# Optimization experiments

Hardware: AMD Instinct MI355X
Metric: run time of the kernel (lower is better)

The kernel has to match this reference:

```python
import jax, jax.numpy as jnp
import numpy as np

N_QUBITS = 4 + 4  # 8
N_LAYERS = 4
DIM = 2 ** N_QUBITS


def _apply_1q(state, U, wire):
    # state: (B, 2,...,2) complex; U: (2,2) complex; contract qubit `wire`
    s = jnp.moveaxis(state, wire + 1, -1)
    s = s @ U.T  # out[..., i] = sum_j U[i, j] * s[..., j]
    return jnp.moveaxis(s, -1, wire + 1)


def _apply_cnot(state, c, t):
    s = jnp.moveaxis(state, (c + 1, t + 1), (-2, -1))  # (..., 2c, 2t)
    s = jnp.concatenate([s[..., 0:1, :], s[..., 1:2, ::-1]], axis=-2)
    return jnp.moveaxis(s, (-2, -1), (c + 1, t + 1))


def _quantum_layer(q_in, qw):
    """Batched statevector sim: RY(pi*x) encoding + StronglyEntanglingLayers + <Z_i>."""
    B = q_in.shape[0]
    # RY(a)|0> = cos(a/2)|0> + sin(a/2)|1>, a = pi * x  -> product state
    half = q_in * (jnp.pi / 2)
    qvecs = jnp.stack([jnp.cos(half), jnp.sin(half)], axis=-1).astype(jnp.complex64)  # (B, n, 2)
    state = qvecs[:, 0]
    for i in range(1, N_QUBITS):
        state = (state[:, :, None] * qvecs[:, i][:, None, :]).reshape(B, -1)
    state = state.reshape((B,) + (2,) * N_QUBITS)
    # Rot(phi, theta, omega) = RZ(omega) RY(theta) RZ(phi)
    phi, theta, omega = qw[..., 0], qw[..., 1], qw[..., 2]
    c, s = jnp.cos(theta / 2), jnp.sin(theta / 2)
    m00 = jnp.exp(-0.5j * (phi + omega)) * c
    m01 = -jnp.exp(0.5j * (phi - omega)) * s
    m10 = jnp.exp(-0.5j * (phi - omega)) * s
    m11 = jnp.exp(0.5j * (phi + omega)) * c
    rot = jnp.stack([jnp.stack([m00, m01], -1), jnp.stack([m10, m11], -1)], -2)  # (L, n, 2, 2)
    rot = rot.astype(jnp.complex64)
    for l in range(N_LAYERS):
        for w in range(N_QUBITS):
            state = _apply_1q(state, rot[l, w], w)
        r = (l % (N_QUBITS - 1)) + 1  # PennyLane default ranges
        for w in range(N_QUBITS):
            state = _apply_cnot(state, w, (w + r) % N_QUBITS)
    amps = state.reshape(B, DIM)
    probs = jnp.real(amps * jnp.conj(amps))  # (B, 2^n) float32
    # <Z_i> = sum_b probs_b * (+1 if bit_i(b)==0 else -1); wire 0 = most significant axis
    idx = np.arange(DIM)
    bits = (idx[None, :] >> (N_QUBITS - 1 - np.arange(N_QUBITS))[:, None]) & 1  # (n, 2^n)
    zvals = jnp.asarray(1.0 - 2.0 * bits, dtype=jnp.float32)
    return probs @ zvals.T  # (B, n)


def _forward(x, w_pre1, b_pre1, w_pre2, b_pre2, w_pre3, b_pre3, qw,
             w_post1, b_post1, w_post2, b_post2, w_post3, b_post3):
    # eval mode: dropout is identity
    h = jax.nn.relu(x @ w_pre1 + b_pre1)
    h = jax.nn.relu(h @ w_pre2 + b_pre2)
    q_in = jnp.tanh(h @ w_pre3 + b_pre3)          # (B, n_qubits)
    z = _quantum_layer(q_in, qw)                   # (B, n_qubits)
    h = jax.nn.relu(z @ w_post1 + b_post1)
    h = jax.nn.relu(h @ w_post2 + b_post2)
    return h @ w_post3 + b_post3                   # (B, num_classes)


def setup_inputs() -> dict:
    key = jax.random.key(0)
    ks = jax.random.split(key, 16)
    B, D_IN, C = 16384, 41, 5
    def lin(k, fan_in, fan_out):
        lim = 1.0 / np.sqrt(fan_in)
        k1, k2 = jax.random.split(k)
        return (jax.random.uniform(k1, (fan_in, fan_out), jnp.float32, -lim, lim),
                jax.random.uniform(k2, (fan_out,), jnp.float32, -lim, lim))
    x = jax.random.normal(ks[0], (B, D_IN), jnp.float32)
    w_pre1, b_pre1 = lin(ks[1], D_IN, 64)
    w_pre2, b_pre2 = lin(ks[2], 64, 32)
    w_pre3, b_pre3 = lin(ks[3], 32, N_QUBITS)
    qw = jax.random.normal(ks[4], (N_LAYERS, N_QUBITS, 3), jnp.float32) * 0.1
    w_post1, b_post1 = lin(ks[5], N_QUBITS, 32)
    w_post2, b_post2 = lin(ks[6], 32, 16)
    w_post3, b_post3 = lin(ks[7], 16, C)
    return dict(x=x, w_pre1=w_pre1, b_pre1=b_pre1, w_pre2=w_pre2, b_pre2=b_pre2,
                w_pre3=w_pre3, b_pre3=b_pre3, qw=qw,
                w_post1=w_post1, b_post1=b_post1, w_post2=w_post2, b_post2=b_post2,
                w_post3=w_post3, b_post3=b_post3)


def reference(x, w_pre1, b_pre1, w_pre2, b_pre2, w_pre3, b_pre3, qw,
              w_post1, b_post1, w_post2, b_post2, w_post3, b_post3):
    return _forward(x, w_pre1, b_pre1, w_pre2, b_pre2, w_pre3, b_pre3, qw,
                    w_post1, b_post1, w_post2, b_post2, w_post3, b_post3)
```

## Files before the change

### kernel.cpp

```cpp
#include <hip/hip_runtime.h>
#include <math.h>

#define PI_HALF 1.57079632679489662f

typedef float v2f __attribute__((ext_vector_type(2)));
typedef unsigned uv2 __attribute__((ext_vector_type(2)));


__device__ __forceinline__ v2f sp(float x) { v2f r; r.x = x; r.y = x; return r; }
__device__ __forceinline__ v2f pkfma(v2f a, v2f b, v2f c) {
  return __builtin_elementwise_fma(a, b, c);
}

template <int CTRL>
__device__ __forceinline__ float dpp_mov(float v) {
  int r = __builtin_amdgcn_update_dpp(0, __float_as_int(v), CTRL, 0xf, 0xf, true);
  return __int_as_float(r);
}

template <int MASK>
__device__ __forceinline__ float lane_xor(float v, bool odd) {
  if constexpr (MASK == 1) return dpp_mov<0xB1>(v);
  else if constexpr (MASK == 2) return dpp_mov<0x4E>(v);
  else if constexpr (MASK == 4) return dpp_mov<0x1B>(dpp_mov<0x141>(v));
  else if constexpr (MASK == 8) return dpp_mov<0x128>(v);
  else {
#if __has_builtin(__builtin_amdgcn_permlane16_swap)
    uv2 r = __builtin_amdgcn_permlane16_swap(__float_as_uint(v),
                                             __float_as_uint(v), false, false);
    return __uint_as_float(odd ? r.x : r.y);
#else
    return __int_as_float(__builtin_amdgcn_ds_swizzle(__float_as_int(v), 0x401F));
#endif
  }
}
template <int MASK>
__device__ __forceinline__ v2f dpp2(v2f v, bool odd) {
  v2f r; r.x = lane_xor<MASK>(v.x, odd); r.y = lane_xor<MASK>(v.y, odd);
  return r;
}

template <int W>
__device__ __forceinline__ void rot_lane(v2f (&RE)[4], v2f (&IM)[4],
                                         const float4 mA, int g) {
  constexpr int LM = 1 << (4 - W);
  const bool odd = (g >> 4) & 1;
  const unsigned bit = (g >> (4 - W)) & 1u;
  const int sgn = (int)(bit << 31);
  v2f Av = sp(mA.x);
  v2f Bv = sp(__int_as_float(__float_as_int(mA.y) ^ sgn));
  v2f Cv = sp(__int_as_float(__float_as_int(mA.z) ^ sgn));
  v2f Dv = sp(mA.w);
#pragma unroll
  for (int j = 0; j < 4; ++j) {
    v2f pr = dpp2<LM>(RE[j], odd);
    v2f pi = dpp2<LM>(IM[j], odd);
    v2f nr = pkfma(-Dv, pi, pkfma(Cv, pr, pkfma(-Bv, IM[j], Av * RE[j])));
    v2f ni = pkfma( Dv, pr, pkfma(Cv, pi, pkfma( Bv, RE[j], Av * IM[j])));
    RE[j] = nr; IM[j] = ni;
  }
}

template <int JM>
__device__ __forceinline__ void rot_regj(v2f (&RE)[4], v2f (&IM)[4],
                                         const float4 mA) {
  v2f M0r = sp(mA.x), M0i = sp(mA.y), M1r = sp(mA.z), M1i = sp(mA.w);
#pragma unroll
  for (int j = 0; j < 4; ++j) {
    if (!(j & JM)) {
      const int j1 = j | JM;
      v2f r0 = RE[j], i0 = IM[j], r1 = RE[j1], i1 = IM[j1];
      RE[j]  = pkfma(-M1i, i1, pkfma(M1r, r1, pkfma(-M0i, i0, M0r * r0)));
      IM[j]  = pkfma( M1i, r1, pkfma(M1r, i1, pkfma( M0i, r0, M0r * i0)));
      RE[j1] = pkfma( M0i, i1, pkfma(M0r, r1, pkfma(-M1i, i0, (-M1r) * r0)));
      IM[j1] = pkfma(-M0i, r1, pkfma(M0r, i1, pkfma( M1i, r0, (-M1r) * i0)));
    }
  }
}

__device__ __forceinline__ void rot_regh(v2f (&RE)[4], v2f (&IM)[4],
                                         const float4 mA) {
#pragma unroll
  for (int j = 0; j < 4; ++j) {
    float r0 = RE[j].x, i0 = IM[j].x, r1 = RE[j].y, i1 = IM[j].y;
    RE[j].x = fmaf(-mA.w, i1, fmaf(mA.z, r1, fmaf(-mA.y, i0, mA.x * r0)));
    IM[j].x = fmaf( mA.w, r1, fmaf(mA.z, i1, fmaf( mA.y, r0, mA.x * i0)));
    RE[j].y = fmaf( mA.y, i1, fmaf(mA.x, r1, fmaf(-mA.w, i0, -mA.z * r0)));
    IM[j].y = fmaf(-mA.y, r1, fmaf(mA.x, i1, fmaf( mA.w, r0, -mA.z * i0)));
  }
}

template <int GPOS, int LM>
__device__ __forceinline__ void cnot_LL(v2f (&RE)[4], v2f (&IM)[4], int g) {
  const bool cb = (g >> GPOS) & 1;
  const bool odd = (g >> 4) & 1;
#pragma unroll
  for (int j = 0; j < 4; ++j) {
    v2f pr = dpp2<LM>(RE[j], odd);
    v2f pi = dpp2<LM>(IM[j], odd);
    RE[j] = cb ? pr : RE[j];
    IM[j] = cb ? pi : IM[j];
  }
}
template <int GPOS, int JM>
__device__ __forceinline__ void cnot_LR(v2f (&RE)[4], v2f (&IM)[4], int g) {
  const bool cb = (g >> GPOS) & 1;
#pragma unroll
  for (int j = 0; j < 4; ++j) {
    if (!(j & JM)) {
      const int j1 = j | JM;
      v2f r0 = RE[j], r1 = RE[j1];
      RE[j] = cb ? r1 : r0;  RE[j1] = cb ? r0 : r1;
      v2f i0 = IM[j], i1 = IM[j1];
      IM[j] = cb ? i1 : i0;  IM[j1] = cb ? i0 : i1;
    }
  }
}
template <int GPOS>
__device__ __forceinline__ void cnot_LH(v2f (&RE)[4], v2f (&IM)[4], int g) {
  const bool cb = (g >> GPOS) & 1;
#pragma unroll
  for (int j = 0; j < 4; ++j) {
    v2f r = RE[j]; v2f rs; rs.x = r.y; rs.y = r.x;
    RE[j] = cb ? rs : r;
    v2f i = IM[j]; v2f is2; is2.x = i.y; is2.y = i.x;
    IM[j] = cb ? is2 : i;
  }
}
template <int JC, int LM>
__device__ __forceinline__ void cnot_RL(v2f (&RE)[4], v2f (&IM)[4], int g) {
  const bool odd = (g >> 4) & 1;
#pragma unroll
  for (int j = 0; j < 4; ++j) {
    if (j & JC) {
      RE[j] = dpp2<LM>(RE[j], odd);
      IM[j] = dpp2<LM>(IM[j], odd);
    }
  }
}
template <int JC>
__device__ __forceinline__ void cnot_RH(v2f (&RE)[4], v2f (&IM)[4]) {
#pragma unroll
  for (int j = 0; j < 4; ++j) {
    if (j & JC) {
      v2f r = RE[j]; RE[j].x = r.y; RE[j].y = r.x;
      v2f i = IM[j]; IM[j].x = i.y; IM[j].y = i.x;
    }
  }
}
template <int LM>
__device__ __forceinline__ void cnot_HL(v2f (&RE)[4], v2f (&IM)[4], int g) {
  const bool odd = (g >> 4) & 1;
#pragma unroll
  for (int j = 0; j < 4; ++j) {
    RE[j].y = lane_xor<LM>(RE[j].y, odd);
    IM[j].y = lane_xor<LM>(IM[j].y, odd);
  }
}
template <int JC, int JT>
__device__ __forceinline__ void cnot_RR(v2f (&RE)[4], v2f (&IM)[4]) {
#pragma unroll
  for (int j = 0; j < 4; ++j) {
    if ((j & JC) && !(j & JT)) {
      const int j1 = j | JT;
      v2f t = RE[j]; RE[j] = RE[j1]; RE[j1] = t;
      t = IM[j]; IM[j] = IM[j1]; IM[j1] = t;
    }
  }
}

__device__ __forceinline__ void stage_fence() { __threadfence_block(); }

__global__ __launch_bounds__(256) void hqc_kernel(
    const float* __restrict__ x,
    const float* __restrict__ w1, const float* __restrict__ b1,
    const float* __restrict__ w2, const float* __restrict__ b2,
    const float* __restrict__ w3, const float* __restrict__ b3,
    const float* __restrict__ qw,
    const float* __restrict__ wp1, const float* __restrict__ bp1,
    const float* __restrict__ wp2, const float* __restrict__ bp2,
    const float* __restrict__ wp3, const float* __restrict__ bp3,
    float* __restrict__ out, int B) {
  __shared__ __align__(16) float rotm[32][4];
  __shared__ float xbuf[8][44];
  __shared__ __align__(16) float hbuf[8][68];
  __shared__ float h2buf[8][34];
  __shared__ float qbuf[8][20];
  __shared__ float p1buf[8][34];
  __shared__ float p2buf[8][20];

  const int tid = threadIdx.x;
  const int g = tid & 31;
  const int ls = tid >> 5;
  const int s = blockIdx.x * 8 + ls;
  const bool valid = (s < B);

  if (tid < 32) {
    float phi = qw[tid * 3 + 0];
    float th  = qw[tid * 3 + 1];
    float om  = qw[tid * 3 + 2];
    float st_, ct; sincosf(0.5f * th, &st_, &ct);
    float sa, ca;  sincosf(0.5f * (phi + om), &sa, &ca);
    float sb, cb;  sincosf(0.5f * (phi - om), &sb, &cb);
    rotm[tid][0] =  ca * ct;
    rotm[tid][1] = -sa * ct;
    rotm[tid][2] = -cb * st_;
    rotm[tid][3] = -sb * st_;
  }

  if (valid) {
    xbuf[ls][g] = x[s * 41 + g];
    if (g < 9) xbuf[ls][g + 32] = x[s * 41 + g + 32];
  }
  __syncthreads();

  const v2f* w1v = (const v2f*)w1;
  v2f a1 = ((const v2f*)b1)[g];
#pragma unroll 8
  for (int k = 0; k < 41; ++k)
    a1 = pkfma(sp(xbuf[ls][k]), w1v[k * 32 + g], a1);
  v2f st2; st2.x = fmaxf(a1.x, 0.f); st2.y = fmaxf(a1.y, 0.f);
  *(v2f*)(&hbuf[ls][2 * g]) = st2;
  stage_fence();

  float a2 = b2[g];
#pragma unroll 8
  for (int k = 0; k < 64; ++k) a2 = fmaf(hbuf[ls][k], w2[k * 32 + g], a2);
  h2buf[ls][g] = fmaxf(a2, 0.f);
  stage_fence();

  if (g < 8) {
    float acc = b3[g];
#pragma unroll
    for (int k = 0; k < 32; ++k) acc = fmaf(h2buf[ls][k], w3[k * 8 + g], acc);
    float q = tanhf(acc);
    float sh, ch; sincosf(q * PI_HALF, &sh, &ch);
    qbuf[ls][g]     = ch;
    qbuf[ls][8 + g] = sh;
  }
  stage_fence();

  float cwv[8], swv[8];
#pragma unroll
  for (int w = 0; w < 8; ++w) { cwv[w] = qbuf[ls][w]; swv[w] = qbuf[ls][8 + w]; }
  float lp = 1.0f;
#pragma unroll
  for (int w = 0; w < 5; ++w) lp *= ((g >> (4 - w)) & 1) ? swv[w] : cwv[w];
  float f56[4];
#pragma unroll
  for (int a = 0; a < 4; ++a)
    f56[a] = ((a & 2) ? swv[5] : cwv[5]) * ((a & 1) ? swv[6] : cwv[6]);
  v2f F7; F7.x = cwv[7]; F7.y = swv[7];
  v2f RE[4], IM[4];
#pragma unroll
  for (int j = 0; j < 4; ++j) {
    RE[j] = sp(lp * f56[j]) * F7;
    IM[j] = sp(0.0f);
  }

#define RM(L, W) (*(const float4*)(&rotm[(L) * 8 + (W)][0]))
#define ROTS(L)                          \
  rot_lane<0>(RE, IM, RM(L, 0), g);      \
  rot_lane<1>(RE, IM, RM(L, 1), g);      \
  rot_lane<2>(RE, IM, RM(L, 2), g);      \
  rot_lane<3>(RE, IM, RM(L, 3), g);      \
  rot_lane<4>(RE, IM, RM(L, 4), g);      \
  rot_regj<2>(RE, IM, RM(L, 5));         \
  rot_regj<1>(RE, IM, RM(L, 6));         \
  rot_regh(RE, IM, RM(L, 7));

  ROTS(0)
  cnot_LL<4, 8>(RE, IM, g);  cnot_LL<3, 4>(RE, IM, g);
  cnot_LL<2, 2>(RE, IM, g);  cnot_LL<1, 1>(RE, IM, g);
  cnot_LR<0, 2>(RE, IM, g);  cnot_RR<2, 1>(RE, IM);
  cnot_RH<1>(RE, IM);        cnot_HL<16>(RE, IM, g);
  ROTS(1)
  cnot_LL<4, 4>(RE, IM, g);  cnot_LL<3, 2>(RE, IM, g);
  cnot_LL<2, 1>(RE, IM, g);  cnot_LR<1, 2>(RE, IM, g);
  cnot_LR<0, 1>(RE, IM, g);  cnot_RH<2>(RE, IM);
  cnot_RL<1, 16>(RE, IM, g); cnot_HL<8>(RE, IM, g);
  ROTS(2)
  cnot_LL<4, 2>(RE, IM, g);  cnot_LL<3, 1>(RE, IM, g);
  cnot_LR<2, 2>(RE, IM, g);  cnot_LR<1, 1>(RE, IM, g);
  cnot_LH<0>(RE, IM, g);     cnot_RL<2, 16>(RE, IM, g);
  cnot_RL<1, 8>(RE, IM, g);  cnot_HL<4>(RE, IM, g);
  ROTS(3)
  cnot_LL<4, 1>(RE, IM, g);  cnot_LR<3, 2>(RE, IM, g);
  cnot_LR<2, 1>(RE, IM, g);  cnot_LH<1>(RE, IM, g);
  cnot_LL<0, 16>(RE, IM, g); cnot_RL<2, 8>(RE, IM, g);
  cnot_RL<1, 4>(RE, IM, g);  cnot_HL<2>(RE, IM, g);

  v2f pv[4];
#pragma unroll
  for (int j = 0; j < 4; ++j) pv[j] = pkfma(RE[j], RE[j], IM[j] * IM[j]);
  v2f tv = (pv[0] + pv[1]) + (pv[2] + pv[3]);
  float tot = tv.x + tv.y;
  v2f v5 = pv[2] + pv[3]; float s5 = v5.x + v5.y;
  v2f v6 = pv[1] + pv[3]; float s6 = v6.x + v6.y;
  float s7 = tv.y;
  float zp[8];
  zp[0] = ((g >> 4) & 1) ? -tot : tot;
  zp[1] = ((g >> 3) & 1) ? -tot : tot;
  zp[2] = ((g >> 2) & 1) ? -tot : tot;
  zp[3] = ((g >> 1) & 1) ? -tot : tot;
  zp[4] = (g & 1) ? -tot : tot;
  zp[5] = fmaf(-2.f, s5, tot);
  zp[6] = fmaf(-2.f, s6, tot);
  zp[7] = fmaf(-2.f, s7, tot);
  {
    const bool odd = (g >> 4) & 1;
#pragma unroll
    for (int w = 0; w < 8; ++w) zp[w] += lane_xor<1>(zp[w], odd);
#pragma unroll
    for (int w = 0; w < 8; ++w) zp[w] += lane_xor<2>(zp[w], odd);
#pragma unroll
    for (int w = 0; w < 8; ++w) zp[w] += lane_xor<4>(zp[w], odd);
#pragma unroll
    for (int w = 0; w < 8; ++w) zp[w] += lane_xor<8>(zp[w], odd);
#pragma unroll
    for (int w = 0; w < 8; ++w) zp[w] += lane_xor<16>(zp[w], odd);
  }

  float q1 = bp1[g];
#pragma unroll
  for (int k = 0; k < 8; ++k) q1 = fmaf(zp[k], wp1[k * 32 + g], q1);
  p1buf[ls][g] = fmaxf(q1, 0.f);
  stage_fence();

  if (g < 16) {
    float q2 = bp2[g];
#pragma unroll
    for (int k = 0; k < 32; ++k) q2 = fmaf(p1buf[ls][k], wp2[k * 16 + g], q2);
    p2buf[ls][g] = fmaxf(q2, 0.f);
  }
  stage_fence();

  if (g < 5 && valid) {
    float o = bp3[g];
#pragma unroll
    for (int k = 0; k < 16; ++k) o = fmaf(p2buf[ls][k], wp3[k * 5 + g], o);
    out[s * 5 + g] = o;
  }
}

extern "C" void kernel_launch(void* const* d_in, const int* in_sizes, int n_in,
                              void* d_out, int out_size, void* d_ws,
                              size_t ws_size, hipStream_t stream) {
  const float* x   = (const float*)d_in[0];
  const float* w1  = (const float*)d_in[1];
  const float* b1  = (const float*)d_in[2];
  const float* w2  = (const float*)d_in[3];
  const float* b2  = (const float*)d_in[4];
  const float* w3  = (const float*)d_in[5];
  const float* b3  = (const float*)d_in[6];
  const float* qw  = (const float*)d_in[7];
  const float* wp1 = (const float*)d_in[8];
  const float* bp1 = (const float*)d_in[9];
  const float* wp2 = (const float*)d_in[10];
  const float* bp2 = (const float*)d_in[11];
  const float* wp3 = (const float*)d_in[12];
  const float* bp3 = (const float*)d_in[13];
  float* out = (float*)d_out;
  const int B = in_sizes[0] / 41;
  const int blocks = (B + 7) / 8;
  hipLaunchKernelGGL(hqc_kernel, dim3(blocks), dim3(256), 0, stream,
                     x, w1, b1, w2, b2, w3, b3, qw,
                     wp1, bp1, wp2, bp2, wp3, bp3, out, B);
}
```

Baseline: 51.72 us.

## Interleave sample pairs in LDS for packed MLP and use masked DPP CNOTs

Shared buffers now interleave the two samples held by each wavefront, so the pre-MLP layers run packed FMAs across two samples, each lane taking one output column (64 wide in layer 1). Controlled-NOTs whose control and target both sit in lane bits now use DPP row/bank write masks, or a single quad permute, in place of a permute followed by a select. Rotation coefficients are loaded before the rotation sequence begins. This is meant to cut VALU select instructions and scalar FMAs, in exchange for more involved DPP mask encodings that must match the qubit mapping exactly.

New measurement: 49.69 us. -3.9%, faster.

```diff
diff --git a/kernel.cpp b/kernel.cpp
--- a/kernel.cpp
+++ b/kernel.cpp
@@ -16,6 +16,22 @@
 __device__ __forceinline__ float dpp_mov(float v) {
   int r = __builtin_amdgcn_update_dpp(0, __float_as_int(v), CTRL, 0xf, 0xf, true);
   return __int_as_float(r);
+}
+template <int CTRL, int ROW, int BANK>
+__device__ __forceinline__ float mdpp(float old_, float src) {
+  int r = __builtin_amdgcn_update_dpp(__float_as_int(old_), __float_as_int(src),
+                                      CTRL, ROW, BANK, false);
+  return __int_as_float(r);
+}
+
+__device__ __forceinline__ float xor16f(float v, bool odd) {
+#if __has_builtin(__builtin_amdgcn_permlane16_swap)
+  uv2 r = __builtin_amdgcn_permlane16_swap(__float_as_uint(v),
+                                           __float_as_uint(v), false, false);
+  return __uint_as_float(odd ? r.x : r.y);
+#else
+  return __int_as_float(__builtin_amdgcn_ds_swizzle(__float_as_int(v), 0x401F));
+#endif
 }
 
 template <int MASK>
@@ -24,15 +40,7 @@
   else if constexpr (MASK == 2) return dpp_mov<0x4E>(v);
   else if constexpr (MASK == 4) return dpp_mov<0x1B>(dpp_mov<0x141>(v));
   else if constexpr (MASK == 8) return dpp_mov<0x128>(v);
-  else {
-#if __has_builtin(__builtin_amdgcn_permlane16_swap)
-    uv2 r = __builtin_amdgcn_permlane16_swap(__float_as_uint(v),
-                                             __float_as_uint(v), false, false);
-    return __uint_as_float(odd ? r.x : r.y);
-#else
-    return __int_as_float(__builtin_amdgcn_ds_swizzle(__float_as_int(v), 0x401F));
-#endif
-  }
+  else return xor16f(v, odd);
 }
 template <int MASK>
 __device__ __forceinline__ v2f dpp2(v2f v, bool odd) {
@@ -90,16 +98,49 @@
   }
 }
 
-template <int GPOS, int LM>
-__device__ __forceinline__ void cnot_LL(v2f (&RE)[4], v2f (&IM)[4], int g) {
+template <int CTRL, int ROW, int BANK>
+__device__ __forceinline__ void cnot_mask(v2f (&RE)[4], v2f (&IM)[4]) {
+#pragma unroll
+  for (int j = 0; j < 4; ++j) {
+    RE[j].x = mdpp<CTRL, ROW, BANK>(RE[j].x, RE[j].x);
+    RE[j].y = mdpp<CTRL, ROW, BANK>(RE[j].y, RE[j].y);
+    IM[j].x = mdpp<CTRL, ROW, BANK>(IM[j].x, IM[j].x);
+    IM[j].y = mdpp<CTRL, ROW, BANK>(IM[j].y, IM[j].y);
+  }
+}
+template <int ROW, int BANK>
+__device__ __forceinline__ void cnot_mask4(v2f (&RE)[4], v2f (&IM)[4]) {
+#pragma unroll
+  for (int j = 0; j < 4; ++j) {
+    float t0 = dpp_mov<0x141>(RE[j].x);
+    float t1 = dpp_mov<0x141>(RE[j].y);
+    float t2 = dpp_mov<0x141>(IM[j].x);
+    float t3 = dpp_mov<0x141>(IM[j].y);
+    RE[j].x = mdpp<0x1B, ROW, BANK>(RE[j].x, t0);
+    RE[j].y = mdpp<0x1B, ROW, BANK>(RE[j].y, t1);
+    IM[j].x = mdpp<0x1B, ROW, BANK>(IM[j].x, t2);
+    IM[j].y = mdpp<0x1B, ROW, BANK>(IM[j].y, t3);
+  }
+}
+__device__ __forceinline__ void cnot_quadB4(v2f (&RE)[4], v2f (&IM)[4]) {
+#pragma unroll
+  for (int j = 0; j < 4; ++j) {
+    RE[j].x = dpp_mov<0xB4>(RE[j].x);
+    RE[j].y = dpp_mov<0xB4>(RE[j].y);
+    IM[j].x = dpp_mov<0xB4>(IM[j].x);
+    IM[j].y = dpp_mov<0xB4>(IM[j].y);
+  }
+}
+template <int GPOS>
+__device__ __forceinline__ void cnot_LL16(v2f (&RE)[4], v2f (&IM)[4], int g) {
   const bool cb = (g >> GPOS) & 1;
   const bool odd = (g >> 4) & 1;
 #pragma unroll
   for (int j = 0; j < 4; ++j) {
-    v2f pr = dpp2<LM>(RE[j], odd);
-    v2f pi = dpp2<LM>(IM[j], odd);
-    RE[j] = cb ? pr : RE[j];
-    IM[j] = cb ? pi : IM[j];
+    float a = xor16f(RE[j].x, odd), b = xor16f(RE[j].y, odd);
+    float c = xor16f(IM[j].x, odd), d = xor16f(IM[j].y, odd);
+    RE[j].x = cb ? a : RE[j].x;  RE[j].y = cb ? b : RE[j].y;
+    IM[j].x = cb ? c : IM[j].x;  IM[j].y = cb ? d : IM[j].y;
   }
 }
 template <int GPOS, int JM>
@@ -121,30 +162,40 @@
   const bool cb = (g >> GPOS) & 1;
 #pragma unroll
   for (int j = 0; j < 4; ++j) {
-    v2f r = RE[j]; v2f rs; rs.x = r.y; rs.y = r.x;
-    RE[j] = cb ? rs : r;
-    v2f i = IM[j]; v2f is2; is2.x = i.y; is2.y = i.x;
-    IM[j] = cb ? is2 : i;
-  }
-}
-template <int JC, int LM>
+    float rx = RE[j].x, ix = IM[j].x;
+    RE[j].x = cb ? RE[j].y : rx;  RE[j].y = cb ? rx : RE[j].y;
+    IM[j].x = cb ? IM[j].y : ix;  IM[j].y = cb ? ix : IM[j].y;
+  }
+}
+template <int JSEL, int LM>
 __device__ __forceinline__ void cnot_RL(v2f (&RE)[4], v2f (&IM)[4], int g) {
   const bool odd = (g >> 4) & 1;
 #pragma unroll
   for (int j = 0; j < 4; ++j) {
-    if (j & JC) {
+    if (j & JSEL) {
       RE[j] = dpp2<LM>(RE[j], odd);
       IM[j] = dpp2<LM>(IM[j], odd);
     }
   }
 }
-template <int JC>
+template <int JSEL>
+__device__ __forceinline__ void cnot_RL16(v2f (&RE)[4], v2f (&IM)[4], int g) {
+  const bool odd = (g >> 4) & 1;
+#pragma unroll
+  for (int j = 0; j < 4; ++j) {
+    if (j & JSEL) {
+      RE[j].x = xor16f(RE[j].x, odd);  RE[j].y = xor16f(RE[j].y, odd);
+      IM[j].x = xor16f(IM[j].x, odd);  IM[j].y = xor16f(IM[j].y, odd);
+    }
+  }
+}
+template <int JSEL>
 __device__ __forceinline__ void cnot_RH(v2f (&RE)[4], v2f (&IM)[4]) {
 #pragma unroll
   for (int j = 0; j < 4; ++j) {
-    if (j & JC) {
-      v2f r = RE[j]; RE[j].x = r.y; RE[j].y = r.x;
-      v2f i = IM[j]; IM[j].x = i.y; IM[j].y = i.x;
+    if (j & JSEL) {
+      float t = RE[j].x; RE[j].x = RE[j].y; RE[j].y = t;
+      t = IM[j].x; IM[j].x = IM[j].y; IM[j].y = t;
     }
   }
 }
@@ -155,6 +206,14 @@
   for (int j = 0; j < 4; ++j) {
     RE[j].y = lane_xor<LM>(RE[j].y, odd);
     IM[j].y = lane_xor<LM>(IM[j].y, odd);
+  }
+}
+__device__ __forceinline__ void cnot_HL16(v2f (&RE)[4], v2f (&IM)[4], int g) {
+  const bool odd = (g >> 4) & 1;
+#pragma unroll
+  for (int j = 0; j < 4; ++j) {
+    RE[j].y = xor16f(RE[j].y, odd);
+    IM[j].y = xor16f(IM[j].y, odd);
   }
 }
 template <int JC, int JT>
@@ -182,17 +241,19 @@
     const float* __restrict__ wp3, const float* __restrict__ bp3,
     float* __restrict__ out, int B) {
   __shared__ __align__(16) float rotm[32][4];
-  __shared__ float xbuf[8][44];
-  __shared__ __align__(16) float hbuf[8][68];
-  __shared__ float h2buf[8][34];
-  __shared__ float qbuf[8][20];
-  __shared__ float p1buf[8][34];
-  __shared__ float p2buf[8][20];
+  __shared__ __align__(8) float xp[4][41][2];
+  __shared__ __align__(8) float hp[4][64][2];
+  __shared__ __align__(8) float h2p[4][32][2];
+  __shared__ __align__(8) float qb[4][16][2];
+  __shared__ __align__(8) float p1p[4][32][2];
+  __shared__ __align__(8) float p2p[4][16][2];
 
   const int tid = threadIdx.x;
+  const int lane = tid & 63;
+  const int wv = tid >> 6;
+  const int half = (tid >> 5) & 1;
   const int g = tid & 31;
-  const int ls = tid >> 5;
-  const int s = blockIdx.x * 8 + ls;
+  const int s = blockIdx.x * 8 + (tid >> 5);
   const bool valid = (s < B);
 
   if (tid < 32) {
@@ -209,40 +270,54 @@
   }
 
   if (valid) {
-    xbuf[ls][g] = x[s * 41 + g];
-    if (g < 9) xbuf[ls][g + 32] = x[s * 41 + g + 32];
+    xp[wv][g][half] = x[s * 41 + g];
+    if (g < 9) xp[wv][g + 32][half] = x[s * 41 + 32 + g];
   }
   __syncthreads();
 
-  const v2f* w1v = (const v2f*)w1;
-  v2f a1 = ((const v2f*)b1)[g];
+  {
+    const int col = lane;
+    v2f acc = sp(b1[col]);
 #pragma unroll 8
-  for (int k = 0; k < 41; ++k)
-    a1 = pkfma(sp(xbuf[ls][k]), w1v[k * 32 + g], a1);
-  v2f st2; st2.x = fmaxf(a1.x, 0.f); st2.y = fmaxf(a1.y, 0.f);
-  *(v2f*)(&hbuf[ls][2 * g]) = st2;
+    for (int k = 0; k < 41; ++k) {
+      v2f xk = *(const v2f*)&xp[wv][k][0];
+      acc = pkfma(xk, sp(w1[k * 64 + col]), acc);
+    }
+    acc.x = fmaxf(acc.x, 0.f); acc.y = fmaxf(acc.y, 0.f);
+    *(v2f*)&hp[wv][col][0] = acc;
+  }
   stage_fence();
 
-  float a2 = b2[g];
+  {
+    v2f acc = sp(b2[g]);
 #pragma unroll 8
-  for (int k = 0; k < 64; ++k) a2 = fmaf(hbuf[ls][k], w2[k * 32 + g], a2);
-  h2buf[ls][g] = fmaxf(a2, 0.f);
+    for (int k = 0; k < 64; ++k) {
+      v2f hk = *(const v2f*)&hp[wv][k][0];
+      acc = pkfma(hk, sp(w2[k * 32 + g]), acc);
+    }
+    acc.x = fmaxf(acc.x, 0.f); acc.y = fmaxf(acc.y, 0.f);
+    if (half == 0) *(v2f*)&h2p[wv][g][0] = acc;
+  }
   stage_fence();
 
   if (g < 8) {
     float acc = b3[g];
 #pragma unroll
-    for (int k = 0; k < 32; ++k) acc = fmaf(h2buf[ls][k], w3[k * 8 + g], acc);
+    for (int k = 0; k < 32; ++k)
+      acc = fmaf(h2p[wv][k][half], w3[k * 8 + g], acc);
     float q = tanhf(acc);
     float sh, ch; sincosf(q * PI_HALF, &sh, &ch);
-    qbuf[ls][g]     = ch;
-    qbuf[ls][8 + g] = sh;
+    qb[wv][g][half]     = ch;
+    qb[wv][8 + g][half] = sh;
   }
   stage_fence();
 
   float cwv[8], swv[8];
 #pragma unroll
-  for (int w = 0; w < 8; ++w) { cwv[w] = qbuf[ls][w]; swv[w] = qbuf[ls][8 + w]; }
+  for (int w = 0; w < 8; ++w) {
+    cwv[w] = qb[wv][w][half];
+    swv[w] = qb[wv][8 + w][half];
+  }
   float lp = 1.0f;
 #pragma unroll
   for (int w = 0; w < 5; ++w) lp *= ((g >> (4 - w)) & 1) ? swv[w] : cwv[w];
@@ -259,36 +334,56 @@
   }
 
 #define RM(L, W) (*(const float4*)(&rotm[(L) * 8 + (W)][0]))
-#define ROTS(L)                          \
-  rot_lane<0>(RE, IM, RM(L, 0), g);      \
-  rot_lane<1>(RE, IM, RM(L, 1), g);      \
-  rot_lane<2>(RE, IM, RM(L, 2), g);      \
-  rot_lane<3>(RE, IM, RM(L, 3), g);      \
-  rot_lane<4>(RE, IM, RM(L, 4), g);      \
-  rot_regj<2>(RE, IM, RM(L, 5));         \
-  rot_regj<1>(RE, IM, RM(L, 6));         \
-  rot_regh(RE, IM, RM(L, 7));
+#define ROTS(L)                                                          \
+  {                                                                      \
+    float4 c0 = RM(L, 0), c1 = RM(L, 1), c2 = RM(L, 2), c3 = RM(L, 3),   \
+           c4 = RM(L, 4), c5 = RM(L, 5), c6 = RM(L, 6), c7 = RM(L, 7);   \
+    rot_lane<0>(RE, IM, c0, g);                                          \
+    rot_lane<1>(RE, IM, c1, g);                                          \
+    rot_lane<2>(RE, IM, c2, g);                                          \
+    rot_lane<3>(RE, IM, c3, g);                                          \
+    rot_lane<4>(RE, IM, c4, g);                                          \
+    rot_regj<2>(RE, IM, c5);                                             \
+    rot_regj<1>(RE, IM, c6);                                             \
+    rot_regh(RE, IM, c7);                                                \
+  }
 
   ROTS(0)
-  cnot_LL<4, 8>(RE, IM, g);  cnot_LL<3, 4>(RE, IM, g);
-  cnot_LL<2, 2>(RE, IM, g);  cnot_LL<1, 1>(RE, IM, g);
-  cnot_LR<0, 2>(RE, IM, g);  cnot_RR<2, 1>(RE, IM);
-  cnot_RH<1>(RE, IM);        cnot_HL<16>(RE, IM, g);
+  cnot_mask<0x128, 0xA, 0xF>(RE, IM);
+  cnot_mask4<0xF, 0xC>(RE, IM);
+  cnot_mask<0x4E, 0xF, 0xA>(RE, IM);
+  cnot_quadB4(RE, IM);
+  cnot_LR<0, 2>(RE, IM, g);
+  cnot_RR<2, 1>(RE, IM);
+  cnot_RH<1>(RE, IM);
+  cnot_HL16(RE, IM, g);
   ROTS(1)
-  cnot_LL<4, 4>(RE, IM, g);  cnot_LL<3, 2>(RE, IM, g);
-  cnot_LL<2, 1>(RE, IM, g);  cnot_LR<1, 2>(RE, IM, g);
-  cnot_LR<0, 1>(RE, IM, g);  cnot_RH<2>(RE, IM);
-  cnot_RL<1, 16>(RE, IM, g); cnot_HL<8>(RE, IM, g);
+  cnot_mask4<0xA, 0xF>(RE, IM);
+  cnot_mask<0x4E, 0xF, 0xC>(RE, IM);
+  cnot_mask<0xB1, 0xF, 0xA>(RE, IM);
+  cnot_LR<1, 2>(RE, IM, g);
+  cnot_LR<0, 1>(RE, IM, g);
+  cnot_RH<2>(RE, IM);
+  cnot_RL16<1>(RE, IM, g);
+  cnot_HL<8>(RE, IM, g);
   ROTS(2)
-  cnot_LL<4, 2>(RE, IM, g);  cnot_LL<3, 1>(RE, IM, g);
-  cnot_LR<2, 2>(RE, IM, g);  cnot_LR<1, 1>(RE, IM, g);
-  cnot_LH<0>(RE, IM, g);     cnot_RL<2, 16>(RE, IM, g);
-  cnot_RL<1, 8>(RE, IM, g);  cnot_HL<4>(RE, IM, g);
+  cnot_mask<0x4E, 0xA, 0xF>(RE, IM);
+  cnot_mask<0xB1, 0xF, 0xC>(RE, IM);
+  cnot_LR<2, 2>(RE, IM, g);
+  cnot_LR<1, 1>(RE, IM, g);
+  cnot_LH<0>(RE, IM, g);
+  cnot_RL16<2>(RE, IM, g);
+  cnot_RL<1, 8>(RE, IM, g);
+  cnot_HL<4>(RE, IM, g);
   ROTS(3)
-  cnot_LL<4, 1>(RE, IM, g);  cnot_LR<3, 2>(RE, IM, g);
-  cnot_LR<2, 1>(RE, IM, g);  cnot_LH<1>(RE, IM, g);
-  cnot_LL<0, 16>(RE, IM, g); cnot_RL<2, 8>(RE, IM, g);
-  cnot_RL<1, 4>(RE, IM, g);  cnot_HL<2>(RE, IM, g);
+  cnot_mask<0xB1, 0xA, 0xF>(RE, IM);
+  cnot_LR<3, 2>(RE, IM, g);
+  cnot_LR<2, 1>(RE, IM, g);
+  cnot_LH<1>(RE, IM, g);
+  cnot_LL16<0>(RE, IM, g);
+  cnot_RL<2, 8>(RE, IM, g);
+  cnot_RL<1, 4>(RE, IM, g);
+  cnot_HL<2>(RE, IM, g);
 
   v2f pv[4];
 #pragma unroll
@@ -321,24 +416,28 @@
     for (int w = 0; w < 8; ++w) zp[w] += lane_xor<16>(zp[w], odd);
   }
 
-  float q1 = bp1[g];
-#pragma unroll
-  for (int k = 0; k < 8; ++k) q1 = fmaf(zp[k], wp1[k * 32 + g], q1);
-  p1buf[ls][g] = fmaxf(q1, 0.f);
+  {
+    float q1 = bp1[g];
+#pragma unroll
+    for (int k = 0; k < 8; ++k) q1 = fmaf(zp[k], wp1[k * 32 + g], q1);
+    p1p[wv][g][half] = fmaxf(q1, 0.f);
+  }
   stage_fence();
 
   if (g < 16) {
     float q2 = bp2[g];
 #pragma unroll
-    for (int k = 0; k < 32; ++k) q2 = fmaf(p1buf[ls][k], wp2[k * 16 + g], q2);
-    p2buf[ls][g] = fmaxf(q2, 0.f);
+    for (int k = 0; k < 32; ++k)
+      q2 = fmaf(p1p[wv][k][half], wp2[k * 16 + g], q2);
+    p2p[wv][g][half] = fmaxf(q2, 0.f);
   }
   stage_fence();
 
   if (g < 5 && valid) {
     float o = bp3[g];
 #pragma unroll
-    for (int k = 0; k < 16; ++k) o = fmaf(p2buf[ls][k], wp3[k * 5 + g], o);
+    for (int k = 0; k < 16; ++k)
+      o = fmaf(p2p[wv][k][half], wp3[k * 5 + g], o);
     out[s * 5 + g] = o;
   }
 }
```
